# Optimization experiments

Hardware: AMD Instinct MI355X
Metric: run time of the kernel (lower is better)

The kernel has to match this reference:

```python
import jax, jax.numpy as jnp
import numpy as np

GRID_SIZE = 128
GAMMA = 200.0


def make_coordinate_grid(dim):
    # meshgrid over [-1, 1] x [-1, 1], shape [G, G, 2] with (x, y) ordering
    x = jnp.arange(dim, dtype=jnp.float32)
    y = jnp.arange(dim, dtype=jnp.float32)
    xx = jnp.broadcast_to(x[None, :], (dim, dim))
    yy = jnp.broadcast_to(y[:, None], (dim, dim))
    meshed = jnp.stack([xx, yy], axis=-1) / (dim - 1) * 2.0 - 1.0
    return meshed  # [G, G, 2]


def distance_transform(kps, mask, grid, gamma):
    # kps: [N, 2] points, mask: [N] bool (True -> segment dropped), grid: [G, G, 2]
    pi = kps[:-1]                      # [S, 2] segment start
    pj = kps[1:]                       # [S, 2] segment end
    v = pi - pj                        # [S, 2]
    u = grid[None, :, :, :] - pj[:, None, None, :]          # [S, G, G, 2]
    uv = jnp.einsum('sghd,sd->sgh', u, v)                   # [S, G, G]
    v_norm = jnp.sum(v * v, axis=-1)                        # [S]
    zero_seg = v_norm == 0.0
    v_safe = jnp.where(zero_seg, 1.0, v_norm)
    # clamp projection to [0,1]; degenerate segments (v_norm==0) fall back to uv
    # (which is exactly 0 there), matching torch's NaN masked_scatter fixup.
    rs = jnp.where(zero_seg[:, None, None], uv,
                   jnp.clip(uv / v_safe[:, None, None], 0.0, 1.0))  # [S, G, G]
    diff = u - rs[..., None] * v[:, None, None, :]          # [S, G, G, 2]
    betas = jnp.exp(-gamma * jnp.sum(diff * diff, axis=-1)) # [S, G, G]
    keep = (~mask[:-1]).astype(betas.dtype)                 # [S]
    betas = betas * keep[:, None, None]
    return jnp.max(betas, axis=0)                           # [G, G]


def setup_inputs() -> dict:
    key = jax.random.key(0)
    k1, k2, k3, k4 = jax.random.split(key, 4)
    N = 2048
    pred_xy = jax.random.uniform(k1, (N, 2), dtype=jnp.float32)
    pred_pen = (jax.random.uniform(k2, (N, 1)) < 0.1).astype(jnp.float32)
    gt_xy = jax.random.uniform(k3, (N, 2), dtype=jnp.float32)
    gt_pen = (jax.random.uniform(k4, (N, 1)) < 0.1).astype(jnp.float32)
    pred_coords = jnp.concatenate([pred_xy, pred_pen], axis=-1)  # [N, 3]
    gt_coords = jnp.concatenate([gt_xy, gt_pen], axis=-1)        # [N, 3]
    return {"pred_coords": pred_coords, "gt_coords": gt_coords}


def reference(pred_coords, gt_coords):
    grid = make_coordinate_grid(GRID_SIZE)
    mask_gt = gt_coords[:, -1] != 0.0
    gt_c = (gt_coords[:, :-1] - 0.5) * 2.0
    mask_pred = pred_coords[:, -1] > 0.5
    pred_c = (pred_coords[:, :-1] - 0.5) * 2.0
    gt_dist = distance_transform(gt_c, mask_gt, grid, GAMMA)
    pred_dist = distance_transform(pred_c, mask_pred, grid, GAMMA)
    dist_loss = jnp.mean((pred_dist - gt_dist) ** 2)
    return dist_loss
```

## Files before the change

kernel.cpp:

```cpp
#include <hip/hip_runtime.h>
#include <math.h>

#define GRID_DIM 128
#define NPIX 16384
#define NSEG 2047
#define NCHUNK 32
#define CHUNK 64
#define NTILE 16
#define GAMMA4 800.0f

typedef float v2f __attribute__((ext_vector_type(2)));


__device__ __forceinline__ void eval2(const v2f gx2, const v2f gy2,
                                      const v2f pjx2, const v2f pjy2,
                                      const v2f bx2, const v2f by2,
                                      const v2f inv2, float& m)
{
    v2f ux = gx2 - pjx2;
    v2f uy = gy2 - pjy2;
    v2f uv = ux * bx2 + uy * by2;
    v2f rs = uv * inv2;
    rs.x = __builtin_amdgcn_fmed3f(rs.x, 0.0f, 1.0f);
    rs.y = __builtin_amdgcn_fmed3f(rs.y, 0.0f, 1.0f);
    v2f dx = ux - rs * bx2;
    v2f dy = uy - rs * by2;
    v2f d2 = dx * dx + dy * dy;
    m = fminf(m, fminf(d2.x, d2.y));
}

__global__ __launch_bounds__(256) void dist_min_kernel(
    const float* __restrict__ pred, const float* __restrict__ gt,
    unsigned int* __restrict__ ws_min)
{
    __shared__ float4 sA[2][CHUNK / 2];
    __shared__ float4 sB[2][CHUNK / 2];
    __shared__ float2 sC[2][CHUNK / 2];

    const int tid = threadIdx.x;
    const int bx = blockIdx.x;
    const int chunk = blockIdx.y;

    if (tid < 2 * CHUNK) {
        const int t = tid >> 6;
        const int sl = tid & (CHUNK - 1);
        const int s = chunk * CHUNK + sl;
        float pjx, pjy, vx, vy, inv;
        if (s < NSEG) {
            const float* src = t ? gt : pred;
            const float pix_ = src[3 * s + 0];
            const float piy_ = src[3 * s + 1];
            const float pen  = src[3 * s + 2];
            pjx = src[3 * s + 3];
            pjy = src[3 * s + 4];
            const bool masked = t ? (pen != 0.0f) : (pen > 0.5f);
            vx = pix_ - pjx;
            vy = piy_ - pjy;
            const float vn = vx * vx + vy * vy;
            inv = (vn == 0.0f) ? 0.0f : (1.0f / vn);
            if (masked) { pjx = 1e15f; pjy = 1e15f; vx = 0.0f; vy = 0.0f; inv = 0.0f; }
        } else {
            pjx = 1e15f; pjy = 1e15f; vx = 0.0f; vy = 0.0f; inv = 0.0f;
        }
        float* a = (float*)&sA[t][sl >> 1];
        float* b = (float*)&sB[t][sl >> 1];
        float* c = (float*)&sC[t][sl >> 1];
        const int k = sl & 1;
        a[k] = pjx; a[2 + k] = pjy;
        b[k] = vx;  b[2 + k] = vy;
        c[k] = inv;
    }
    __syncthreads();

    const int p0 = bx * 1024 + tid;
    const int p1 = p0 + 256;
    const int p2 = p0 + 512;
    const int p3 = p0 + 768;
    const float gx0 = (float)(p0 & (GRID_DIM - 1)) * (1.0f / 127.0f);
    const float gy0 = (float)(p0 >> 7) * (1.0f / 127.0f);
    const float gx1 = (float)(p1 & (GRID_DIM - 1)) * (1.0f / 127.0f);
    const float gy1 = (float)(p1 >> 7) * (1.0f / 127.0f);
    const float gx2_ = (float)(p2 & (GRID_DIM - 1)) * (1.0f / 127.0f);
    const float gy2_ = (float)(p2 >> 7) * (1.0f / 127.0f);
    const float gx3 = (float)(p3 & (GRID_DIM - 1)) * (1.0f / 127.0f);
    const float gy3 = (float)(p3 >> 7) * (1.0f / 127.0f);
    const v2f gx20 = {gx0, gx0}, gy20 = {gy0, gy0};
    const v2f gx21 = {gx1, gx1}, gy21 = {gy1, gy1};
    const v2f gx22 = {gx2_, gx2_}, gy22 = {gy2_, gy2_};
    const v2f gx23 = {gx3, gx3}, gy23 = {gy3, gy3};

    #pragma unroll
    for (int t = 0; t < 2; ++t) {
        float m0 = 3.0e38f, m1 = 3.0e38f, m2 = 3.0e38f, m3 = 3.0e38f;
        #pragma unroll
        for (int i = 0; i < CHUNK / 2; ++i) {
            const float4 A = sA[t][i];
            const float4 B = sB[t][i];
            const float2 C = sC[t][i];
            const v2f bx2 = {B.x, B.y}, by2 = {B.z, B.w};
            const v2f pjx2 = {A.x, A.y}, pjy2 = {A.z, A.w};
            const v2f inv2 = {C.x, C.y};
            eval2(gx20, gy20, pjx2, pjy2, bx2, by2, inv2, m0);
            eval2(gx21, gy21, pjx2, pjy2, bx2, by2, inv2, m1);
            eval2(gx22, gy22, pjx2, pjy2, bx2, by2, inv2, m2);
            eval2(gx23, gy23, pjx2, pjy2, bx2, by2, inv2, m3);
        }
        atomicMin(&ws_min[t * NPIX + p0], __float_as_uint(m0));
        atomicMin(&ws_min[t * NPIX + p1], __float_as_uint(m1));
        atomicMin(&ws_min[t * NPIX + p2], __float_as_uint(m2));
        atomicMin(&ws_min[t * NPIX + p3], __float_as_uint(m3));
    }
}

__global__ __launch_bounds__(256) void dist_reduce_kernel(
    const uint4* __restrict__ ws_min, float* __restrict__ out)
{
    __shared__ float s_part[4];
    const int tid = threadIdx.x;
    const int q = blockIdx.x * 256 + tid;
    const uint4 bp = ws_min[q];
    const uint4 bg = ws_min[(NPIX / 4) + q];
    float acc;
    {
        const float d0 = __expf(-GAMMA4 * __uint_as_float(bp.x))
                       - __expf(-GAMMA4 * __uint_as_float(bg.x));
        const float d1 = __expf(-GAMMA4 * __uint_as_float(bp.y))
                       - __expf(-GAMMA4 * __uint_as_float(bg.y));
        const float d2 = __expf(-GAMMA4 * __uint_as_float(bp.z))
                       - __expf(-GAMMA4 * __uint_as_float(bg.z));
        const float d3 = __expf(-GAMMA4 * __uint_as_float(bp.w))
                       - __expf(-GAMMA4 * __uint_as_float(bg.w));
        acc = d0 * d0 + d1 * d1 + d2 * d2 + d3 * d3;
    }
    #pragma unroll
    for (int off = 32; off > 0; off >>= 1)
        acc += __shfl_down(acc, off, 64);
    if ((tid & 63) == 0) s_part[tid >> 6] = acc;
    __syncthreads();
    if (tid == 0) {
        const float blk = (s_part[0] + s_part[1] + s_part[2] + s_part[3])
                          * (1.0f / (float)NPIX);
        atomicAdd(out, blk);
    }
}

extern "C" void kernel_launch(void* const* d_in, const int* in_sizes, int n_in,
                              void* d_out, int out_size, void* d_ws, size_t ws_size,
                              hipStream_t stream)
{
    const float* pred = (const float*)d_in[0];
    const float* gt   = (const float*)d_in[1];

    dim3 grid(NTILE, NCHUNK);
    dist_min_kernel<<<grid, 256, 0, stream>>>(pred, gt, (unsigned int*)d_ws);

    dist_reduce_kernel<<<NPIX / 4 / 256, 256, 0, stream>>>(
        (const uint4*)d_ws, (float*)d_out);
}
```

Measured before the change: 69.23 us.

## Cull segments outside each tile's row band using ballot compaction

Each block now keeps only the segments that are unmasked and whose y-extent overlaps the block's 8-row band widened by a cull radius. Survivors are packed into shared memory with a wavefront ballot and prefix popcount, with an odd-count pad entry. The inner loop runs a dynamic trip count instead of a fully unrolled fixed one. The goal is to skip distance work for far-away and masked segments. In exchange it loses the compile-time unroll and drops contributions beyond the radius, which are bounded by about exp(-18).

```diff
diff --git a/kernel.cpp b/kernel.cpp
--- a/kernel.cpp
+++ b/kernel.cpp
@@ -8,6 +8,7 @@
 #define CHUNK 64
 #define NTILE 16
 #define GAMMA4 800.0f
+#define CULL_R 0.15f
 
 typedef float v2f __attribute__((ext_vector_type(2)));
 
@@ -36,6 +37,7 @@
     __shared__ float4 sA[2][CHUNK / 2];
     __shared__ float4 sB[2][CHUNK / 2];
     __shared__ float2 sC[2][CHUNK / 2];
+    __shared__ int    sCnt[2];
 
     const int tid = threadIdx.x;
     const int bx = blockIdx.x;
@@ -45,7 +47,8 @@
         const int t = tid >> 6;
         const int sl = tid & (CHUNK - 1);
         const int s = chunk * CHUNK + sl;
-        float pjx, pjy, vx, vy, inv;
+        bool keep = false;
+        float pjx = 0.0f, pjy = 0.0f, vx = 0.0f, vy = 0.0f, inv = 0.0f;
         if (s < NSEG) {
             const float* src = t ? gt : pred;
             const float pix_ = src[3 * s + 0];
@@ -54,21 +57,38 @@
             pjx = src[3 * s + 3];
             pjy = src[3 * s + 4];
             const bool masked = t ? (pen != 0.0f) : (pen > 0.5f);
+            const float ylo = (float)(bx * 8)     * (1.0f / 127.0f) - CULL_R;
+            const float yhi = (float)(bx * 8 + 7) * (1.0f / 127.0f) + CULL_R;
+            keep = !masked && (fmaxf(piy_, pjy) >= ylo)
+                           && (fminf(piy_, pjy) <= yhi);
             vx = pix_ - pjx;
             vy = piy_ - pjy;
             const float vn = vx * vx + vy * vy;
             inv = (vn == 0.0f) ? 0.0f : (1.0f / vn);
-            if (masked) { pjx = 1e15f; pjy = 1e15f; vx = 0.0f; vy = 0.0f; inv = 0.0f; }
-        } else {
-            pjx = 1e15f; pjy = 1e15f; vx = 0.0f; vy = 0.0f; inv = 0.0f;
         }
-        float* a = (float*)&sA[t][sl >> 1];
-        float* b = (float*)&sB[t][sl >> 1];
-        float* c = (float*)&sC[t][sl >> 1];
-        const int k = sl & 1;
-        a[k] = pjx; a[2 + k] = pjy;
-        b[k] = vx;  b[2 + k] = vy;
-        c[k] = inv;
+        const unsigned long long bal = __ballot(keep);
+        const int k   = __popcll(bal & ((1ull << sl) - 1ull));
+        const int cnt = __popcll(bal);
+        if (keep) {
+            float* a = (float*)&sA[t][k >> 1];
+            float* b = (float*)&sB[t][k >> 1];
+            float* c = (float*)&sC[t][k >> 1];
+            const int e = k & 1;
+            a[e] = pjx; a[2 + e] = pjy;
+            b[e] = vx;  b[2 + e] = vy;
+            c[e] = inv;
+        }
+        if (sl == 0) {
+            sCnt[t] = (cnt + 1) >> 1;
+            if (cnt & 1) {
+                float* a = (float*)&sA[t][cnt >> 1];
+                float* b = (float*)&sB[t][cnt >> 1];
+                float* c = (float*)&sC[t][cnt >> 1];
+                a[1] = 1e15f; a[3] = 1e15f;
+                b[1] = 0.0f;  b[3] = 0.0f;
+                c[1] = 0.0f;
+            }
+        }
     }
     __syncthreads();
 
@@ -91,9 +111,9 @@
 
     #pragma unroll
     for (int t = 0; t < 2; ++t) {
+        const int np = sCnt[t];
         float m0 = 3.0e38f, m1 = 3.0e38f, m2 = 3.0e38f, m3 = 3.0e38f;
-        #pragma unroll
-        for (int i = 0; i < CHUNK / 2; ++i) {
+        for (int i = 0; i < np; ++i) {
             const float4 A = sA[t][i];
             const float4 B = sB[t][i];
             const float2 C = sC[t][i];
```

Measured after the change: 66.01 us. -4.7%, faster.
